# Kernel optimization log

Hardware: AMD Instinct MI355X
Metric: run time of the kernel (lower is better)

Reference implementation:

```python
import jax, jax.numpy as jnp
import numpy as np

N_NODES = 50000
N_EDGES = 800000
IN_CH = 128
OUT_CH = 64
HEADS = 4
NEG_SLOPE = 0.2


def setup_inputs() -> dict:
    key = jax.random.key(0)
    k1, k2, k3, k4, k5 = jax.random.split(key, 5)
    x = jax.random.normal(k1, (N_NODES, IN_CH), dtype=jnp.float32)
    edge_index = jax.random.randint(k2, (2, N_EDGES), 0, N_NODES, dtype=jnp.int64)
    # Glorot-ish scaled params
    W = jax.random.normal(k3, (IN_CH, HEADS * OUT_CH), dtype=jnp.float32) * (1.0 / np.sqrt(IN_CH))
    att_src = jax.random.normal(k4, (HEADS, OUT_CH), dtype=jnp.float32) * (1.0 / np.sqrt(OUT_CH))
    att_dst = jax.random.normal(k5, (HEADS, OUT_CH), dtype=jnp.float32) * (1.0 / np.sqrt(OUT_CH))
    bias = jnp.zeros((HEADS * OUT_CH,), dtype=jnp.float32)
    return {"x": x, "edge_index": edge_index, "W": W, "att_src": att_src, "att_dst": att_dst, "bias": bias}


def reference(x, edge_index, W, att_src, att_dst, bias):
    N = x.shape[0]
    H, C = att_src.shape
    # PyG GATConv default add_self_loops=True
    loops = jnp.arange(N, dtype=edge_index.dtype)
    src = jnp.concatenate([edge_index[0], loops])  # message source j
    dst = jnp.concatenate([edge_index[1], loops])  # message target i
    # Linear transform per head: [N, H, C]
    h = (x @ W).reshape(N, H, C)
    # Per-node attention logits: [N, H]
    a_src = jnp.sum(h * att_src[None], axis=-1)
    a_dst = jnp.sum(h * att_dst[None], axis=-1)
    # Per-edge raw score (alpha_src from source node, alpha_dst from target node)
    e = jax.nn.leaky_relu(a_src[src] + a_dst[dst], NEG_SLOPE)  # [E, H]
    # Segment-softmax over incoming edges of each target node
    m = jax.ops.segment_max(e, dst, num_segments=N)  # [N, H]
    m = jnp.where(jnp.isfinite(m), m, 0.0)  # nodes with no edges -> 0
    ex = jnp.exp(e - m[dst])
    denom = jax.ops.segment_sum(ex, dst, num_segments=N)  # [N, H]
    alpha = ex / (denom[dst] + 1e-16)  # [E, H]
    # Weighted aggregate of source features: [N, H, C]
    msg = h[src] * alpha[:, :, None]
    out = jax.ops.segment_sum(msg, dst, num_segments=N)
    # concat=True: flatten heads, add bias
    return out.reshape(N, H * C) + bias
```

## Files before the change

### kernel.cpp

```cpp
#include <hip/hip_runtime.h>

#define N_NODES 50000
#define N_EDGES 800000
#define IN_CH 128
#define OUT_CH 64
#define HEADS 4
#define HC 256
#define NEG_SLOPE 0.2f
#define GEMM_BLOCKS 782
#define COUNT_BLOCKS 782
#define SCAN_BLOCKS 49

#define HB_OFF       0UL
#define WSW_OFF      25600000UL
#define ASRC_OFF     25665536UL
#define ADST_OFF     26465536UL
#define COUNTS_OFF   27265536UL
#define OFFSETS_OFF  27465536UL
#define CURSOR_OFF   27665536UL
#define BSUMS_OFF    27865536UL
#define REC_OFF      27866560UL

typedef __attribute__((ext_vector_type(8))) short short8;
typedef __attribute__((ext_vector_type(4))) float f32x4;

__device__ __forceinline__ unsigned short f2bf(float f) {
  unsigned int u = __float_as_uint(f);
  unsigned int r = (u + 0x7fffu + ((u >> 16) & 1u)) >> 16;
  return (unsigned short)r;
}
__device__ __forceinline__ float bf2f_lo(unsigned int u) {
  return __uint_as_float(u << 16);
}
__device__ __forceinline__ float bf2f_hi(unsigned int u) {
  return __uint_as_float(u & 0xffff0000u);
}
__device__ __forceinline__ float lrelu(float e) {
  return e > 0.f ? e : NEG_SLOPE * e;
}

__global__ __launch_bounds__(256) void init_k(const float* __restrict__ W,
                                              unsigned short* __restrict__ Wsw,
                                              int* __restrict__ counts) {
  if (blockIdx.x < 16) {
    int idx = blockIdx.x * 256 + threadIdx.x;
    int l = idx & 63;
    int kc = (idx >> 6) & 3;
    int t = idx >> 8;
    int kbase = kc * 32 + (l >> 4) * 8;
    int col = t * 16 + (l & 15);
    unsigned int p[4];
#pragma unroll
    for (int j = 0; j < 4; ++j) {
      unsigned int lo = f2bf(W[(size_t)(kbase + 2 * j) * HC + col]);
      unsigned int hi = f2bf(W[(size_t)(kbase + 2 * j + 1) * HC + col]);
      p[j] = lo | (hi << 16);
    }
    *(uint4*)(Wsw + (size_t)idx * 8) = make_uint4(p[0], p[1], p[2], p[3]);
  } else {
    int i = (blockIdx.x - 16) * 256 + threadIdx.x;
    if (i < N_NODES) counts[i] = 0;
  }
}

__global__ __launch_bounds__(256) void gemm_count(const float* __restrict__ x,
                                                  const unsigned short* __restrict__ Wsw,
                                                  const float* __restrict__ att_s,
                                                  const float* __restrict__ att_d,
                                                  const int* __restrict__ dstv,
                                                  unsigned short* __restrict__ hb,
                                                  float* __restrict__ a_src,
                                                  float* __restrict__ a_dst,
                                                  int* __restrict__ counts) {
  __shared__ float Cs[4][16][256];

  if (blockIdx.x >= GEMM_BLOCKS) {
    int base = (blockIdx.x - GEMM_BLOCKS) * 1024 + threadIdx.x;
#pragma unroll
    for (int k = 0; k < 4; ++k) {
      int e = base + k * 256;
      if (e < N_EDGES) atomicAdd(&counts[dstv[e]], 1);
    }
    return;
  }

  const int wave = threadIdx.x >> 6;
  const int l = threadIdx.x & 63;
  const int q = l >> 4;
  const int m = l & 15;
  const int mrow = blockIdx.x * 64 + wave * 16 + m;
  const bool mvalid = mrow < N_NODES;
  const int rc = mvalid ? mrow : (N_NODES - 1);

  short8 a[4];
  const float* xr = x + (size_t)rc * IN_CH + q * 8;
#pragma unroll
  for (int kc = 0; kc < 4; ++kc) {
    float4 u = *(const float4*)(xr + kc * 32);
    float4 v = *(const float4*)(xr + kc * 32 + 4);
    short8 t;
    t[0] = (short)f2bf(u.x); t[1] = (short)f2bf(u.y);
    t[2] = (short)f2bf(u.z); t[3] = (short)f2bf(u.w);
    t[4] = (short)f2bf(v.x); t[5] = (short)f2bf(v.y);
    t[6] = (short)f2bf(v.z); t[7] = (short)f2bf(v.w);
    a[kc] = t;
  }

#pragma unroll
  for (int t = 0; t < 16; ++t) {
    f32x4 acc = {0.f, 0.f, 0.f, 0.f};
#pragma unroll
    for (int kc = 0; kc < 4; ++kc) {
      short8 b = *(const short8*)(Wsw + ((size_t)(t * 4 + kc) * 64 + l) * 8);
      acc = __builtin_amdgcn_mfma_f32_16x16x32_bf16(a[kc], b, acc, 0, 0, 0);
    }
#pragma unroll
    for (int r = 0; r < 4; ++r) {
      int row = q * 4 + r;
      Cs[wave][row][(t * 16 + m) ^ (row << 2)] = acc[r];
    }
  }
  __syncthreads();

  float as = 0.f, ad = 0.f;
  unsigned short* hrow = hb + (size_t)mrow * HC + q * 64;
  const int sw = m << 2;
#pragma unroll
  for (int i = 0; i < 8; ++i) {
    int col0 = q * 64 + i * 8;
    float4 c1 = *(const float4*)&Cs[wave][m][(col0) ^ sw];
    float4 c2 = *(const float4*)&Cs[wave][m][(col0 + 4) ^ sw];
    float4 s1 = *(const float4*)(att_s + col0);
    float4 s2 = *(const float4*)(att_s + col0 + 4);
    float4 d1 = *(const float4*)(att_d + col0);
    float4 d2 = *(const float4*)(att_d + col0 + 4);
    as += c1.x * s1.x + c1.y * s1.y + c1.z * s1.z + c1.w * s1.w;
    as += c2.x * s2.x + c2.y * s2.y + c2.z * s2.z + c2.w * s2.w;
    ad += c1.x * d1.x + c1.y * d1.y + c1.z * d1.z + c1.w * d1.w;
    ad += c2.x * d2.x + c2.y * d2.y + c2.z * d2.z + c2.w * d2.w;
    if (mvalid) {
      uint4 p;
      p.x = (unsigned int)f2bf(c1.x) | ((unsigned int)f2bf(c1.y) << 16);
      p.y = (unsigned int)f2bf(c1.z) | ((unsigned int)f2bf(c1.w) << 16);
      p.z = (unsigned int)f2bf(c2.x) | ((unsigned int)f2bf(c2.y) << 16);
      p.w = (unsigned int)f2bf(c2.z) | ((unsigned int)f2bf(c2.w) << 16);
      *(uint4*)(hrow + i * 8) = p;
    }
  }
  if (mvalid) {
    a_src[mrow * HEADS + q] = as;
    a_dst[mrow * HEADS + q] = ad;
  }
}

__global__ __launch_bounds__(256) void scan1(const int* __restrict__ counts,
                                             int* __restrict__ offsets,
                                             int* __restrict__ bsums) {
  __shared__ int sd[256];
  const int base = blockIdx.x * 1024;
  const int t = threadIdx.x;
  int v[4];
  int tsum = 0;
#pragma unroll
  for (int k = 0; k < 4; ++k) {
    int i = base + t * 4 + k;
    v[k] = (i < N_NODES) ? counts[i] : 0;
    tsum += v[k];
  }
  sd[t] = tsum;
  __syncthreads();
  for (int off = 1; off < 256; off <<= 1) {
    int xval = (t >= off) ? sd[t - off] : 0;
    __syncthreads();
    sd[t] += xval;
    __syncthreads();
  }
  int excl = sd[t] - tsum;
  int run = excl;
#pragma unroll
  for (int k = 0; k < 4; ++k) {
    int i = base + t * 4 + k;
    if (i < N_NODES) offsets[i] = run;
    run += v[k];
  }
  if (t == 255) bsums[blockIdx.x] = sd[255];
}

__global__ __launch_bounds__(256) void scan23(int* __restrict__ offsets,
                                              const int* __restrict__ bsums,
                                              int* __restrict__ cursor) {
  __shared__ int s_add;
  if (threadIdx.x < 64) {
    int lane = threadIdx.x;
    int v = (lane < SCAN_BLOCKS) ? bsums[lane] : 0;
#pragma unroll
    for (int o = 1; o < 64; o <<= 1) {
      int t = __shfl_up(v, o);
      if (lane >= o) v += t;
    }
    int b = blockIdx.x;
    int pre = (b == 0) ? 0 : __shfl(v, b - 1);
    if (lane == 0) s_add = pre;
  }
  __syncthreads();
  const int add = s_add;
  const int base = blockIdx.x * 1024;
  const int t = threadIdx.x;
#pragma unroll
  for (int k = 0; k < 4; ++k) {
    int i = base + t * 4 + k;
    if (i < N_NODES) {
      int o = offsets[i] + add;
      offsets[i] = o;
      cursor[i] = o;
    }
  }
}

__global__ __launch_bounds__(256) void scatter_k(const int* __restrict__ src,
                                                 const int* __restrict__ dst,
                                                 const float* __restrict__ a_src,
                                                 const float* __restrict__ a_dst,
                                                 int* __restrict__ cursor,
                                                 char* __restrict__ rec) {
  int e = blockIdx.x * 256 + threadIdx.x;
  if (e < N_EDGES) {
    int s = src[e];
    int d = dst[e];
    float4 as = *(const float4*)(a_src + s * 4);
    float4 ad = *(const float4*)(a_dst + d * 4);
    float4 ex;
    ex.x = __expf(lrelu(as.x + ad.x));
    ex.y = __expf(lrelu(as.y + ad.y));
    ex.z = __expf(lrelu(as.z + ad.z));
    ex.w = __expf(lrelu(as.w + ad.w));
    int pos = atomicAdd(&cursor[d], 1);
    char* rp = rec + (size_t)pos * 32;
    *(uint4*)rp = make_uint4((unsigned)s, __float_as_uint(ex.x),
                             __float_as_uint(ex.y), __float_as_uint(ex.z));
    *(unsigned*)(rp + 16) = __float_as_uint(ex.w);
  }
}

__global__ __launch_bounds__(256) void aggregate(const unsigned short* __restrict__ hb,
                                                 const float* __restrict__ a_src,
                                                 const float* __restrict__ a_dst,
                                                 const int* __restrict__ counts,
                                                 const int* __restrict__ offsets,
                                                 const char* __restrict__ rec,
                                                 const float* __restrict__ bias,
                                                 float* __restrict__ out) {
  const int node = blockIdx.x * 4 + (threadIdx.x >> 6);
  const int l = threadIdx.x & 63;
  const int g = l >> 4;
  const int q = l & 15;
  const int hd = q >> 2;
  const int cb = q * 32;
  const int deg = counts[node];
  const int start = offsets[node];
  const char* hbase = (const char*)hb;

  float denom = 0.f;
  float acc[16];
#pragma unroll
  for (int k = 0; k < 16; ++k) acc[k] = 0.f;

#pragma unroll 2
  for (int j = 0; j + g < deg; j += 4) {
    int idx = start + j + g;
    const char* rp = rec + (size_t)idx * 32;
    int s = *(const int*)rp;
    float ex = *(const float*)(rp + 4 + hd * 4);
    const char* hp = hbase + (size_t)s * 512 + cb;
    uint4 h0 = *(const uint4*)hp;
    uint4 h1 = *(const uint4*)(hp + 16);
    denom += ex;
    acc[0] += bf2f_lo(h0.x) * ex;  acc[1] += bf2f_hi(h0.x) * ex;
    acc[2] += bf2f_lo(h0.y) * ex;  acc[3] += bf2f_hi(h0.y) * ex;
    acc[4] += bf2f_lo(h0.z) * ex;  acc[5] += bf2f_hi(h0.z) * ex;
    acc[6] += bf2f_lo(h0.w) * ex;  acc[7] += bf2f_hi(h0.w) * ex;
    acc[8] += bf2f_lo(h1.x) * ex;  acc[9] += bf2f_hi(h1.x) * ex;
    acc[10] += bf2f_lo(h1.y) * ex; acc[11] += bf2f_hi(h1.y) * ex;
    acc[12] += bf2f_lo(h1.z) * ex; acc[13] += bf2f_hi(h1.z) * ex;
    acc[14] += bf2f_lo(h1.w) * ex; acc[15] += bf2f_hi(h1.w) * ex;
  }

  denom += __shfl_xor(denom, 16);
  denom += __shfl_xor(denom, 32);
#pragma unroll
  for (int k = 0; k < 16; ++k) {
    acc[k] += __shfl_xor(acc[k], 16);
    acc[k] += __shfl_xor(acc[k], 32);
  }

  float es = a_src[node * HEADS + hd] + a_dst[node * HEADS + hd];
  float exs = __expf(lrelu(es));
  denom += exs;
  const char* hp = hbase + (size_t)node * 512 + cb;
  uint4 h0 = *(const uint4*)hp;
  uint4 h1 = *(const uint4*)(hp + 16);
  acc[0] += bf2f_lo(h0.x) * exs;  acc[1] += bf2f_hi(h0.x) * exs;
  acc[2] += bf2f_lo(h0.y) * exs;  acc[3] += bf2f_hi(h0.y) * exs;
  acc[4] += bf2f_lo(h0.z) * exs;  acc[5] += bf2f_hi(h0.z) * exs;
  acc[6] += bf2f_lo(h0.w) * exs;  acc[7] += bf2f_hi(h0.w) * exs;
  acc[8] += bf2f_lo(h1.x) * exs;  acc[9] += bf2f_hi(h1.x) * exs;
  acc[10] += bf2f_lo(h1.y) * exs; acc[11] += bf2f_hi(h1.y) * exs;
  acc[12] += bf2f_lo(h1.z) * exs; acc[13] += bf2f_hi(h1.z) * exs;
  acc[14] += bf2f_lo(h1.w) * exs; acc[15] += bf2f_hi(h1.w) * exs;

  float inv = 1.f / (denom + 1e-16f);
  int c = q * 16 + g * 4;
  float4 bv = *(const float4*)(bias + c);
  float4 o = make_float4(acc[g * 4 + 0] * inv + bv.x, acc[g * 4 + 1] * inv + bv.y,
                         acc[g * 4 + 2] * inv + bv.z, acc[g * 4 + 3] * inv + bv.w);
  *(float4*)(out + (size_t)node * HC + c) = o;
}

extern "C" void kernel_launch(void* const* d_in, const int* in_sizes, int n_in,
                              void* d_out, int out_size, void* d_ws, size_t ws_size,
                              hipStream_t stream) {
  const float* x     = (const float*)d_in[0];
  const int*   ei    = (const int*)d_in[1];
  const float* W     = (const float*)d_in[2];
  const float* att_s = (const float*)d_in[3];
  const float* att_d = (const float*)d_in[4];
  const float* bias  = (const float*)d_in[5];
  float* out = (float*)d_out;

  char* ws = (char*)d_ws;
  unsigned short* hb  = (unsigned short*)(ws + HB_OFF);
  unsigned short* Wsw = (unsigned short*)(ws + WSW_OFF);
  float* a_src  = (float*)(ws + ASRC_OFF);
  float* a_dst  = (float*)(ws + ADST_OFF);
  int* counts   = (int*)(ws + COUNTS_OFF);
  int* offsets  = (int*)(ws + OFFSETS_OFF);
  int* cursor   = (int*)(ws + CURSOR_OFF);
  int* bsums    = (int*)(ws + BSUMS_OFF);
  char* rec     = (char*)(ws + REC_OFF);

  const int* src = ei;
  const int* dst = ei + N_EDGES;

  init_k<<<16 + 196, 256, 0, stream>>>(W, Wsw, counts);
  gemm_count<<<GEMM_BLOCKS + COUNT_BLOCKS, 256, 0, stream>>>(
      x, Wsw, att_s, att_d, dst, hb, a_src, a_dst, counts);
  scan1<<<SCAN_BLOCKS, 256, 0, stream>>>(counts, offsets, bsums);
  scan23<<<SCAN_BLOCKS, 256, 0, stream>>>(offsets, bsums, cursor);
  scatter_k<<<3125, 256, 0, stream>>>(src, dst, a_src, a_dst, cursor, rec);
  aggregate<<<12500, 256, 0, stream>>>(hb, a_src, a_dst, counts, offsets, rec, bias, out);
}
```

Measured before the change: 249.8 us.

## Store features as fp16, split edge records into SoA, and batch two gathers

Stores the transformed node features as packed fp16 instead of bf16, using the hardware packed round-toward-zero convert so the aggregation decodes them with a direct half-to-float conversion. The padded 32-byte per-edge record becomes two separate arrays, a source index and a float4 of exponentials, which cuts the bytes written and read per edge. The aggregation loop now fetches two edges per iteration per lane group to keep more independent loads in flight. fp16 has a narrower range than bf16, and the extra live registers may lower occupancy.

```diff
diff --git a/kernel.cpp b/kernel.cpp
--- a/kernel.cpp
+++ b/kernel.cpp
@@ -19,21 +19,26 @@
 #define OFFSETS_OFF  27465536UL
 #define CURSOR_OFF   27665536UL
 #define BSUMS_OFF    27865536UL
-#define REC_OFF      27866560UL
+#define SIDX_OFF     27866560UL
+#define EXV_OFF      31066560UL
 
 typedef __attribute__((ext_vector_type(8))) short short8;
 typedef __attribute__((ext_vector_type(4))) float f32x4;
+typedef __attribute__((ext_vector_type(2))) __fp16 fp16x2;
 
 __device__ __forceinline__ unsigned short f2bf(float f) {
   unsigned int u = __float_as_uint(f);
   unsigned int r = (u + 0x7fffu + ((u >> 16) & 1u)) >> 16;
   return (unsigned short)r;
 }
-__device__ __forceinline__ float bf2f_lo(unsigned int u) {
-  return __uint_as_float(u << 16);
-}
-__device__ __forceinline__ float bf2f_hi(unsigned int u) {
-  return __uint_as_float(u & 0xffff0000u);
+__device__ __forceinline__ unsigned f2h2(float a, float b) {
+  fp16x2 h = __builtin_amdgcn_cvt_pkrtz(a, b);
+  return __builtin_bit_cast(unsigned, h);
+}
+__device__ __forceinline__ void fma2(float& a0, float& a1, unsigned u, float e) {
+  fp16x2 h = __builtin_bit_cast(fp16x2, u);
+  a0 = fmaf((float)h.x, e, a0);
+  a1 = fmaf((float)h.y, e, a1);
 }
 __device__ __forceinline__ float lrelu(float e) {
   return e > 0.f ? e : NEG_SLOPE * e;
@@ -140,10 +145,10 @@
     ad += c2.x * d2.x + c2.y * d2.y + c2.z * d2.z + c2.w * d2.w;
     if (mvalid) {
       uint4 p;
-      p.x = (unsigned int)f2bf(c1.x) | ((unsigned int)f2bf(c1.y) << 16);
-      p.y = (unsigned int)f2bf(c1.z) | ((unsigned int)f2bf(c1.w) << 16);
-      p.z = (unsigned int)f2bf(c2.x) | ((unsigned int)f2bf(c2.y) << 16);
-      p.w = (unsigned int)f2bf(c2.z) | ((unsigned int)f2bf(c2.w) << 16);
+      p.x = f2h2(c1.x, c1.y);
+      p.y = f2h2(c1.z, c1.w);
+      p.z = f2h2(c2.x, c2.y);
+      p.w = f2h2(c2.z, c2.w);
       *(uint4*)(hrow + i * 8) = p;
     }
   }
@@ -222,7 +227,8 @@
                                                  const float* __restrict__ a_src,
                                                  const float* __restrict__ a_dst,
                                                  int* __restrict__ cursor,
-                                                 char* __restrict__ rec) {
+                                                 int* __restrict__ sidx,
+                                                 float* __restrict__ exv) {
   int e = blockIdx.x * 256 + threadIdx.x;
   if (e < N_EDGES) {
     int s = src[e];
@@ -235,10 +241,8 @@
     ex.z = __expf(lrelu(as.z + ad.z));
     ex.w = __expf(lrelu(as.w + ad.w));
     int pos = atomicAdd(&cursor[d], 1);
-    char* rp = rec + (size_t)pos * 32;
-    *(uint4*)rp = make_uint4((unsigned)s, __float_as_uint(ex.x),
-                             __float_as_uint(ex.y), __float_as_uint(ex.z));
-    *(unsigned*)(rp + 16) = __float_as_uint(ex.w);
+    sidx[pos] = s;
+    *(float4*)(exv + (size_t)pos * 4) = ex;
   }
 }
 
@@ -247,7 +251,8 @@
                                                  const float* __restrict__ a_dst,
                                                  const int* __restrict__ counts,
                                                  const int* __restrict__ offsets,
-                                                 const char* __restrict__ rec,
+                                                 const int* __restrict__ sidx,
+                                                 const float* __restrict__ exv,
                                                  const float* __restrict__ bias,
                                                  float* __restrict__ out) {
   const int node = blockIdx.x * 4 + (threadIdx.x >> 6);
@@ -265,24 +270,29 @@
 #pragma unroll
   for (int k = 0; k < 16; ++k) acc[k] = 0.f;
 
-#pragma unroll 2
-  for (int j = 0; j + g < deg; j += 4) {
-    int idx = start + j + g;
-    const char* rp = rec + (size_t)idx * 32;
-    int s = *(const int*)rp;
-    float ex = *(const float*)(rp + 4 + hd * 4);
-    const char* hp = hbase + (size_t)s * 512 + cb;
-    uint4 h0 = *(const uint4*)hp;
-    uint4 h1 = *(const uint4*)(hp + 16);
-    denom += ex;
-    acc[0] += bf2f_lo(h0.x) * ex;  acc[1] += bf2f_hi(h0.x) * ex;
-    acc[2] += bf2f_lo(h0.y) * ex;  acc[3] += bf2f_hi(h0.y) * ex;
-    acc[4] += bf2f_lo(h0.z) * ex;  acc[5] += bf2f_hi(h0.z) * ex;
-    acc[6] += bf2f_lo(h0.w) * ex;  acc[7] += bf2f_hi(h0.w) * ex;
-    acc[8] += bf2f_lo(h1.x) * ex;  acc[9] += bf2f_hi(h1.x) * ex;
-    acc[10] += bf2f_lo(h1.y) * ex; acc[11] += bf2f_hi(h1.y) * ex;
-    acc[12] += bf2f_lo(h1.z) * ex; acc[13] += bf2f_hi(h1.z) * ex;
-    acc[14] += bf2f_lo(h1.w) * ex; acc[15] += bf2f_hi(h1.w) * ex;
+  for (int j = 0; j + g < deg; j += 8) {
+    int i0 = start + j + g;
+    bool v1 = (j + g + 4) < deg;
+    int i1 = v1 ? (i0 + 4) : i0;
+    int s0 = sidx[i0];
+    int s1 = sidx[i1];
+    float ex0 = exv[(size_t)i0 * 4 + hd];
+    float ex1 = v1 ? exv[(size_t)i1 * 4 + hd] : 0.f;
+    const char* hp0 = hbase + (size_t)s0 * 512 + cb;
+    const char* hp1 = hbase + (size_t)s1 * 512 + cb;
+    uint4 A0 = *(const uint4*)hp0;
+    uint4 A1 = *(const uint4*)(hp0 + 16);
+    uint4 B0 = *(const uint4*)hp1;
+    uint4 B1 = *(const uint4*)(hp1 + 16);
+    denom += ex0 + ex1;
+    fma2(acc[0],  acc[1],  A0.x, ex0);  fma2(acc[2],  acc[3],  A0.y, ex0);
+    fma2(acc[4],  acc[5],  A0.z, ex0);  fma2(acc[6],  acc[7],  A0.w, ex0);
+    fma2(acc[8],  acc[9],  A1.x, ex0);  fma2(acc[10], acc[11], A1.y, ex0);
+    fma2(acc[12], acc[13], A1.z, ex0);  fma2(acc[14], acc[15], A1.w, ex0);
+    fma2(acc[0],  acc[1],  B0.x, ex1);  fma2(acc[2],  acc[3],  B0.y, ex1);
+    fma2(acc[4],  acc[5],  B0.z, ex1);  fma2(acc[6],  acc[7],  B0.w, ex1);
+    fma2(acc[8],  acc[9],  B1.x, ex1);  fma2(acc[10], acc[11], B1.y, ex1);
+    fma2(acc[12], acc[13], B1.z, ex1);  fma2(acc[14], acc[15], B1.w, ex1);
   }
 
   denom += __shfl_xor(denom, 16);
@@ -299,14 +309,10 @@
   const char* hp = hbase + (size_t)node * 512 + cb;
   uint4 h0 = *(const uint4*)hp;
   uint4 h1 = *(const uint4*)(hp + 16);
-  acc[0] += bf2f_lo(h0.x) * exs;  acc[1] += bf2f_hi(h0.x) * exs;
-  acc[2] += bf2f_lo(h0.y) * exs;  acc[3] += bf2f_hi(h0.y) * exs;
-  acc[4] += bf2f_lo(h0.z) * exs;  acc[5] += bf2f_hi(h0.z) * exs;
-  acc[6] += bf2f_lo(h0.w) * exs;  acc[7] += bf2f_hi(h0.w) * exs;
-  acc[8] += bf2f_lo(h1.x) * exs;  acc[9] += bf2f_hi(h1.x) * exs;
-  acc[10] += bf2f_lo(h1.y) * exs; acc[11] += bf2f_hi(h1.y) * exs;
-  acc[12] += bf2f_lo(h1.z) * exs; acc[13] += bf2f_hi(h1.z) * exs;
-  acc[14] += bf2f_lo(h1.w) * exs; acc[15] += bf2f_hi(h1.w) * exs;
+  fma2(acc[0],  acc[1],  h0.x, exs);  fma2(acc[2],  acc[3],  h0.y, exs);
+  fma2(acc[4],  acc[5],  h0.z, exs);  fma2(acc[6],  acc[7],  h0.w, exs);
+  fma2(acc[8],  acc[9],  h1.x, exs);  fma2(acc[10], acc[11], h1.y, exs);
+  fma2(acc[12], acc[13], h1.z, exs);  fma2(acc[14], acc[15], h1.w, exs);
 
   float inv = 1.f / (denom + 1e-16f);
   int c = q * 16 + g * 4;
@@ -336,7 +342,8 @@
   int* offsets  = (int*)(ws + OFFSETS_OFF);
   int* cursor   = (int*)(ws + CURSOR_OFF);
   int* bsums    = (int*)(ws + BSUMS_OFF);
-  char* rec     = (char*)(ws + REC_OFF);
+  int* sidx     = (int*)(ws + SIDX_OFF);
+  float* exv    = (float*)(ws + EXV_OFF);
 
   const int* src = ei;
   const int* dst = ei + N_EDGES;
@@ -346,6 +353,6 @@
       x, Wsw, att_s, att_d, dst, hb, a_src, a_dst, counts);
   scan1<<<SCAN_BLOCKS, 256, 0, stream>>>(counts, offsets, bsums);
   scan23<<<SCAN_BLOCKS, 256, 0, stream>>>(offsets, bsums, cursor);
-  scatter_k<<<3125, 256, 0, stream>>>(src, dst, a_src, a_dst, cursor, rec);
-  aggregate<<<12500, 256, 0, stream>>>(hb, a_src, a_dst, counts, offsets, rec, bias, out);
-}
+  scatter_k<<<3125, 256, 0, stream>>>(src, dst, a_src, a_dst, cursor, sidx, exv);
+  aggregate<<<12500, 256, 0, stream>>>(hb, a_src, a_dst, counts, offsets, sidx, exv, bias, out);
+}
```

After: 246.9 us. No clear change (-1.1%).
